# Performance work log

Hardware: AMD Instinct MI355X
Metric: run time of the kernel (lower is better)

The kernel has to match this reference:

```python
import jax, jax.numpy as jnp
import numpy as np

N_Q = 5000
MEM = 50
KDIM = 50
VDIM = 200
FC = 50
B = 2048
S = 200


def setup_inputs() -> dict:
    key = jax.random.key(0)
    ks = jax.random.split(key, 14)
    inp = {}
    inp["q_data"] = jax.random.randint(ks[0], (B, S), 0, N_Q, dtype=jnp.int64)
    inp["qa_data"] = jax.random.randint(ks[1], (B, S), 0, 2 * N_Q, dtype=jnp.int64)
    # learned parameters (kaiming-ish random init)
    inp["q_embed_w"] = jax.random.normal(ks[2], (N_Q + 1, KDIM), jnp.float32) * 0.2
    inp["qa_embed_w"] = jax.random.normal(ks[3], (2 * N_Q + 1, VDIM), jnp.float32) * 0.1
    inp["key_memory"] = jax.random.normal(ks[4], (MEM, KDIM), jnp.float32) * 0.2
    inp["init_value_memory"] = jax.random.normal(ks[5], (MEM, VDIM), jnp.float32) * 0.1
    # DKVMN write gates: erase (sigmoid) and add (tanh) transforms of qa embedding
    inp["erase_w"] = jax.random.normal(ks[6], (VDIM, VDIM), jnp.float32) * 0.1
    inp["erase_b"] = jnp.zeros((VDIM,), jnp.float32)
    inp["add_w"] = jax.random.normal(ks[7], (VDIM, VDIM), jnp.float32) * 0.1
    inp["add_b"] = jnp.zeros((VDIM,), jnp.float32)
    # prediction MLP: Linear(VDIM+KDIM -> FC), Tanh, Linear(FC -> 1)
    inp["pred_w1"] = jax.random.normal(ks[8], (VDIM + KDIM, FC), jnp.float32) * 0.1
    inp["pred_b1"] = jnp.zeros((FC,), jnp.float32)
    inp["pred_w2"] = jax.random.normal(ks[9], (FC, 1), jnp.float32) * 0.2
    inp["pred_b2"] = jnp.zeros((1,), jnp.float32)
    return inp


def _dkvmn_forward(q_data, qa_data, q_embed_w, qa_embed_w, key_memory,
                   init_value_memory, erase_w, erase_b, add_w, add_b,
                   pred_w1, pred_b1, pred_w2, pred_b2):
    q_emb = q_embed_w[q_data]    # [B, S, KDIM]
    qa_emb = qa_embed_w[qa_data]  # [B, S, VDIM]
    batch = q_data.shape[0]
    Mv0 = jnp.broadcast_to(init_value_memory, (batch, MEM, VDIM))

    def step(Mv, xs):
        q_t, qa_t = xs  # [B, KDIM], [B, VDIM]
        # attention over memory slots
        w = jax.nn.softmax(q_t @ key_memory.T, axis=-1)          # [B, MEM]
        read = jnp.einsum('bm,bmv->bv', w, Mv)                    # [B, VDIM]
        h = jnp.tanh(jnp.concatenate([read, q_t], -1) @ pred_w1 + pred_b1)
        p = jax.nn.sigmoid((h @ pred_w2 + pred_b2)[:, 0])         # [B]
        # erase/add write
        e = jax.nn.sigmoid(qa_t @ erase_w + erase_b)              # [B, VDIM]
        a = jnp.tanh(qa_t @ add_w + add_b)                        # [B, VDIM]
        Mv_new = Mv * (1.0 - w[:, :, None] * e[:, None, :]) + w[:, :, None] * a[:, None, :]
        return Mv_new, p

    xs = (jnp.swapaxes(q_emb, 0, 1), jnp.swapaxes(qa_emb, 0, 1))  # time-major
    _, preds = jax.lax.scan(step, Mv0, xs)                        # [S, B]
    return preds.T                                                # [B, S]


def reference(q_data, qa_data, q_embed_w, qa_embed_w, key_memory,
              init_value_memory, erase_w, erase_b, add_w, add_b,
              pred_w1, pred_b1, pred_w2, pred_b2):
    preds = _dkvmn_forward(q_data, qa_data, q_embed_w, qa_embed_w, key_memory,
                           init_value_memory, erase_w, erase_b, add_w, add_b,
                           pred_w1, pred_b1, pred_w2, pred_b2)
    zeros = jnp.zeros_like(preds)
    return (preds, zeros, zeros, zeros)
```

## Files before the change

### kernel.cpp

```cpp
#include <hip/hip_runtime.h>
#include <hip/hip_fp16.h>


#define NQ1   5001
#define NQA   10001
#define MEMN  50
#define KD    50
#define VD    200
#define FC    50
#define BB    2048
#define SS    200
#define EA_R  16
#define WHS   28

#define EA_B   626
#define WQ_B   1251
#define PACK_B 8
#define PREP_G (EA_B + WQ_B + PACK_B)

typedef unsigned int   u32;
typedef unsigned short u16;
typedef short    s8v __attribute__((ext_vector_type(8)));
typedef float    f4v __attribute__((ext_vector_type(4)));
typedef _Float16 h2v __attribute__((ext_vector_type(2)));

__device__ __forceinline__ float fast_sigmoid(float x) { return 1.f / (1.f + __expf(-x)); }
__device__ __forceinline__ float fast_tanh(float x) {
    float e2 = __expf(2.f * x);
    return 1.f - 2.f / (e2 + 1.f);
}
__device__ __forceinline__ float bfu16_to_f(u16 u) {
    union { float f; u32 i; } x; x.i = ((u32)u) << 16; return x.f;
}
__device__ __forceinline__ u16 f_to_bfu16(float f) {
    union { float f; u32 i; } x; x.f = f;
    return (u16)((x.i + 0x7fffu + ((x.i >> 16) & 1u)) >> 16);
}
__device__ __forceinline__ h2v u32_to_h2v(u32 u) {
    union { u32 i; h2v h; } x; x.i = u; return x.h;
}
__device__ __forceinline__ u16 f16bits(float f) {
    union { __half h; u16 u; } x; x.h = __float2half(f); return x.u;
}
__device__ __forceinline__ float h16_to_f(u16 u) {
    union { u16 u; __half h; } x; x.u = u; return __half2float(x.h);
}

__global__ __launch_bounds__(256) void prep(
        const float* __restrict__ qemb, const float* __restrict__ km,
        const float* __restrict__ w1,   const float* __restrict__ b1,
        const float* __restrict__ qaemb,
        const float* __restrict__ ew,   const float* __restrict__ ebias,
        const float* __restrict__ aw,   const float* __restrict__ abias,
        float* __restrict__ Wt, u32* __restrict__ Wh, float* __restrict__ Q1,
        u32* __restrict__ EA, u16* __restrict__ W1s,
        float* __restrict__ out_aux) {
    const int tid = threadIdx.x;
    const int blk = blockIdx.x;

    for (size_t i = (size_t)blk * 256 + tid; i < 3ull * BB * SS;
         i += (size_t)PREP_G * 256)
        out_aux[i] = 0.f;

    __shared__ float smem[VD * EA_R];

    if (blk < EA_B) {
        const int r0 = blk * EA_R;
        if (tid < VD) {
            #pragma unroll
            for (int r = 0; r < EA_R; ++r) {
                int row = r0 + r;
                smem[tid * EA_R + r] = (row < NQA) ? qaemb[(size_t)row * VD + tid] : 0.f;
            }
        }
        __syncthreads();
        if (tid >= VD) return;

        float accE[EA_R], accA[EA_R];
        #pragma unroll
        for (int r = 0; r < EA_R; ++r) { accE[r] = 0.f; accA[r] = 0.f; }
        for (int k = 0; k < VD; ++k) {
            float we = ew[k * VD + tid];
            float wa = aw[k * VD + tid];
            #pragma unroll
            for (int r = 0; r < EA_R; ++r) {
                float qv = smem[k * EA_R + r];
                accE[r] = fmaf(qv, we, accE[r]);
                accA[r] = fmaf(qv, wa, accA[r]);
            }
        }
        float be = ebias[tid], ba = abias[tid];
        #pragma unroll
        for (int r = 0; r < EA_R; ++r) {
            int row = r0 + r;
            if (row < NQA) {
                u16 ne16 = f16bits(-fast_sigmoid(accE[r] + be));
                u16 a16  = f16bits(fast_tanh(accA[r] + ba));
                EA[(size_t)row * VD + tid] = (u32)ne16 | ((u32)a16 << 16);
            }
        }
    } else if (blk < EA_B + WQ_B) {
        const int lane = tid & 63;
        const int wv   = tid >> 6;
        const int q    = (blk - EA_B) * 4 + wv;
        const bool qok = q < NQ1;
        float* qrow = smem + wv * 64;
        if (qok && lane < KD) qrow[lane] = qemb[q * KD + lane];
        __syncthreads();
        if (!qok) return;

        float s = -1e30f;
        if (lane < MEMN) {
            s = 0.f;
            #pragma unroll
            for (int k = 0; k < KD; ++k) s = fmaf(qrow[k], km[lane * KD + k], s);
        }
        float mx = s;
        #pragma unroll
        for (int off = 32; off >= 1; off >>= 1) mx = fmaxf(mx, __shfl_xor(mx, off, 64));
        float e = (lane < MEMN) ? __expf(s - mx) : 0.f;
        float sum = e;
        #pragma unroll
        for (int off = 32; off >= 1; off >>= 1) sum += __shfl_xor(sum, off, 64);
        float wv_ = (lane < MEMN) ? (e / sum) : 0.f;
        if (lane < MEMN) Wt[q * MEMN + lane] = wv_;

        float plo = __shfl(wv_, 2 * (lane & 31), 64);
        float phi = __shfl(wv_, 2 * (lane & 31) + 1, 64);
        if (lane < 25) {
            Wh[q * WHS + lane] = (u32)f16bits(plo) | ((u32)f16bits(phi) << 16);
        } else if (lane < WHS) {
            Wh[q * WHS + lane] = 0;
        }

        if (lane < FC) {
            float h = b1[lane];
            #pragma unroll
            for (int k = 0; k < KD; ++k)
                h = fmaf(qrow[k], w1[(VD + k) * FC + lane], h);
            Q1[q * FC + lane] = h;
        }
    } else {
        for (int idx = (blk - EA_B - WQ_B) * 256 + tid; idx < 4 * 7 * 64 * 8;
             idx += PACK_B * 256) {
            int j    = idx & 7;
            int lane = (idx >> 3) & 63;
            int kt   = (idx >> 9) % 7;
            int nt   = idx / 3584;
            int k = kt * 32 + ((lane >> 4) << 3) + j;
            int n = nt * 16 + (lane & 15);
            float v = (k < VD && n < FC) ? w1[k * FC + n] : 0.f;
            W1s[idx] = f_to_bfu16(v);
        }
    }
}

__global__ __launch_bounds__(256) void dkvmn_state(
        const int* __restrict__ qd, const int* __restrict__ qad,
        const u32* __restrict__ Wh, const u32* __restrict__ EA,
        const float* __restrict__ ivm, u16* __restrict__ READ) {
    const int tid = threadIdx.x;
    const int b   = blockIdx.x;
    const int v   = tid;
    const bool active = v < VD;
    const int vc = active ? v : VD - 1;

    h2v mv[25];
    #pragma unroll
    for (int i = 0; i < 25; ++i) {
        mv[i].x = (_Float16)ivm[(2 * i) * VD + vc];
        mv[i].y = (_Float16)ivm[(2 * i + 1) * VD + vc];
    }

    const int base = b * SS;
    int q_c = __builtin_amdgcn_readfirstlane(qd[base]);
    int q_n = __builtin_amdgcn_readfirstlane(qd[base + 1]);
    int qa0 = __builtin_amdgcn_readfirstlane(qad[base]);
    int qa1 = __builtin_amdgcn_readfirstlane(qad[base + 1]);
    u32 ea_c = EA[(size_t)qa0 * VD + vc];
    u32 ea_n = EA[(size_t)qa1 * VD + vc];

    for (int t = 0; t < SS; ++t) {
        int tn = t + 2; tn = (tn < SS) ? tn : (SS - 1);
        int q_nn  = __builtin_amdgcn_readfirstlane(qd[base + tn]);
        int qa_nn = __builtin_amdgcn_readfirstlane(qad[base + tn]);
        u32 ea_nn = EA[(size_t)qa_nn * VD + vc];

        const u32* wrow = Wh + q_c * WHS;
        h2v nev2 = u32_to_h2v(__builtin_amdgcn_perm(ea_c, ea_c, 0x01000100u));
        h2v av2  = u32_to_h2v(__builtin_amdgcn_perm(ea_c, ea_c, 0x03020302u));

        float rdA = 0.f, rdB = 0.f;
        #pragma unroll
        for (int i = 0; i < 25; i += 2) {
            h2v w0 = u32_to_h2v(wrow[i]);
#if __has_builtin(__builtin_amdgcn_fdot2)
            rdA = __builtin_amdgcn_fdot2(w0, mv[i], rdA, false);
#else
            rdA = fmaf((float)w0.x, (float)mv[i].x,
                  fmaf((float)w0.y, (float)mv[i].y, rdA));
#endif
            mv[i] = __builtin_elementwise_fma(
                w0, __builtin_elementwise_fma(nev2, mv[i], av2), mv[i]);
            if (i + 1 < 25) {
                h2v w1p = u32_to_h2v(wrow[i + 1]);
#if __has_builtin(__builtin_amdgcn_fdot2)
                rdB = __builtin_amdgcn_fdot2(w1p, mv[i + 1], rdB, false);
#else
                rdB = fmaf((float)w1p.x, (float)mv[i + 1].x,
                      fmaf((float)w1p.y, (float)mv[i + 1].y, rdB));
#endif
                mv[i + 1] = __builtin_elementwise_fma(
                    w1p, __builtin_elementwise_fma(nev2, mv[i + 1], av2), mv[i + 1]);
            }
        }
        if (active)
            READ[(size_t)(base + t) * VD + v] = f_to_bfu16(rdA + rdB);
        q_c = q_n; q_n = q_nn; ea_c = ea_n; ea_n = ea_nn;
    }
}

__global__ __launch_bounds__(256) void mlp_pred(
        const u16* __restrict__ RD, const int* __restrict__ qd,
        const float* __restrict__ Q1tab, const u16* __restrict__ W1s,
        const float* __restrict__ w2, const float* __restrict__ b2,
        float* __restrict__ out) {
    const int tid  = threadIdx.x;
    const int lane = tid & 63;
    const int wv   = tid >> 6;
    const int strip = blockIdx.x * 4 + wv;
    const int row0  = strip * 16;

    const int mrow = lane & 15;
    const int quad = lane >> 4;

    s8v a[7];
    {
        const u16* arow = RD + (size_t)(row0 + mrow) * VD + quad * 8;
        #pragma unroll
        for (int kt = 0; kt < 7; ++kt)
            a[kt] = *(const s8v*)(arow + kt * 32);
    }

    const float b2f = b2[0];
    float pf[4] = {0.f, 0.f, 0.f, 0.f};

    #pragma unroll
    for (int nt = 0; nt < 4; ++nt) {
        s8v bfr[7];
        #pragma unroll
        for (int kt = 0; kt < 7; ++kt)
            bfr[kt] = *(const s8v*)(W1s + (((nt * 7 + kt) * 64) + lane) * 8);

        f4v acc = {0.f, 0.f, 0.f, 0.f};
        #pragma unroll
        for (int kt = 0; kt < 7; ++kt)
            acc = __builtin_amdgcn_mfma_f32_16x16x32_bf16(a[kt], bfr[kt], acc, 0, 0, 0);

        const int f = nt * 16 + mrow;
        const float w2f = (f < FC) ? w2[f] : 0.f;
        #pragma unroll
        for (int r = 0; r < 4; ++r) {
            int row = row0 + quad * 4 + r;
            float h = acc[r] + Q1tab[qd[row] * FC + f];
            pf[r] = fmaf(fast_tanh(h), w2f, pf[r]);
        }
    }

    #pragma unroll
    for (int r = 0; r < 4; ++r) {
        float s = pf[r];
        s += __shfl_xor(s, 1, 64);
        s += __shfl_xor(s, 2, 64);
        s += __shfl_xor(s, 4, 64);
        s += __shfl_xor(s, 8, 64);
        if (mrow == 0)
            out[row0 + quad * 4 + r] = fast_sigmoid(s + b2f);
    }
}

__global__ void dkvmn_main(const int* __restrict__ qd, const int* __restrict__ qad,
                           const float* __restrict__ Wtab, const float* __restrict__ Q1tab,
                           const u32* __restrict__ EA,
                           const float* __restrict__ ivm,
                           const float* __restrict__ w1,
                           const float* __restrict__ w2,
                           const float* __restrict__ b2,
                           float* __restrict__ out) {
    const int tid  = threadIdx.x;
    const int b    = blockIdx.x;
    const int v    = tid;
    const int lane = tid & 63;
    const int wv   = tid >> 6;

    __shared__ alignas(16) float read_lds[4 * 52];
    __shared__ alignas(16) float part_lds[4 * 52];

    float mv[MEMN];
    if (v < VD) {
        #pragma unroll
        for (int m = 0; m < MEMN; ++m) mv[m] = ivm[m * VD + v];
    }
    float w1r[50];
    if (lane < FC) {
        #pragma unroll
        for (int i = 0; i < 50; ++i) w1r[i] = w1[(wv * 50 + i) * FC + lane];
    } else {
        #pragma unroll
        for (int i = 0; i < 50; ++i) w1r[i] = 0.f;
    }
    const float w2f = (tid < FC) ? w2[tid] : 0.f;
    const float b2f = b2[0];

    const int* qrow_i  = qd  + b * SS;
    const int* qarow_i = qad + b * SS;
    const int jchunk = v / 50;
    const int wslot  = jchunk * 52 + (v - jchunk * 50);

    for (int t = 0; t < SS; ++t) {
        const int q  = __builtin_amdgcn_readfirstlane(qrow_i[t]);
        const int qa = __builtin_amdgcn_readfirstlane(qarow_i[t]);
        const float* wrow = Wtab + q * MEMN;

        u32 ea = 0;
        if (v < VD) ea = EA[(size_t)qa * VD + v];
        float ne = h16_to_f((u16)(ea & 0xffffu));
        float av = h16_to_f((u16)(ea >> 16));

        if (v < VD) {
            float rd0 = 0.f, rd1 = 0.f;
            #pragma unroll
            for (int m = 0; m < MEMN; m += 2) {
                float wm0 = wrow[m], wm1 = wrow[m + 1];
                rd0 = fmaf(wm0, mv[m], rd0);
                mv[m] = fmaf(wm0, fmaf(ne, mv[m], av), mv[m]);
                rd1 = fmaf(wm1, mv[m + 1], rd1);
                mv[m + 1] = fmaf(wm1, fmaf(ne, mv[m + 1], av), mv[m + 1]);
            }
            read_lds[wslot] = rd0 + rd1;
        }
        __syncthreads();

        float part = 0.f;
        {
            const float* rlc = read_lds + wv * 52;
            #pragma unroll
            for (int i = 0; i < 48; i += 4) {
                float4 x = *(const float4*)(rlc + i);
                part = fmaf(x.x, w1r[i],     part);
                part = fmaf(x.y, w1r[i + 1], part);
                part = fmaf(x.z, w1r[i + 2], part);
                part = fmaf(x.w, w1r[i + 3], part);
            }
            part = fmaf(rlc[48], w1r[48], part);
            part = fmaf(rlc[49], w1r[49], part);
        }
        if (lane < FC) part_lds[wv * 52 + lane] = part;
        __syncthreads();

        if (wv == 0) {
            float pf = 0.f;
            if (lane < FC) {
                float h = part_lds[lane] + part_lds[52 + lane] +
                          part_lds[104 + lane] + part_lds[156 + lane] +
                          Q1tab[q * FC + lane];
                pf = fast_tanh(h) * w2f;
            }
            #pragma unroll
            for (int off = 32; off >= 1; off >>= 1) pf += __shfl_xor(pf, off, 64);
            if (lane == 0) out[b * SS + t] = fast_sigmoid(pf + b2f);
        }
    }
}

extern "C" void kernel_launch(void* const* d_in, const int* in_sizes, int n_in,
                              void* d_out, int out_size, void* d_ws, size_t ws_size,
                              hipStream_t stream) {
    const int* qd  = (const int*)d_in[0];
    const int* qad = (const int*)d_in[1];
    const float* qemb  = (const float*)d_in[2];
    const float* qaemb = (const float*)d_in[3];
    const float* km    = (const float*)d_in[4];
    const float* ivm   = (const float*)d_in[5];
    const float* ew    = (const float*)d_in[6];
    const float* eb    = (const float*)d_in[7];
    const float* aw    = (const float*)d_in[8];
    const float* ab    = (const float*)d_in[9];
    const float* w1    = (const float*)d_in[10];
    const float* b1    = (const float*)d_in[11];
    const float* w2    = (const float*)d_in[12];
    const float* b2    = (const float*)d_in[13];
    float* out = (float*)d_out;
    (void)in_sizes; (void)n_in; (void)out_size;

    char* ws = (char*)d_ws;
    float* Wt  = (float*)(ws);
    float* Q1  = (float*)(ws + 1000448);
    u32*   EA  = (u32*)  (ws + 2000896);
    u16*   W1s = (u16*)  (ws + 10001920);
    u32*   Wh  = (u32*)  (ws + 10034688);
    u16*   RD  = (u16*)  (ws + 10595328);
    const size_t need = 10595328ull + 163840000ull + 512ull;

    prep<<<PREP_G, 256, 0, stream>>>(qemb, km, w1, b1, qaemb, ew, eb, aw, ab,
                                     Wt, Wh, Q1, EA, W1s, out + (size_t)BB * SS);

    if (ws_size >= need) {
        dkvmn_state<<<BB, 256, 0, stream>>>(qd, qad, Wh, EA, ivm, RD);
        mlp_pred<<<(BB * SS) / 64, 256, 0, stream>>>(RD, qd, Q1, W1s, w2, b2, out);
    } else {
        dkvmn_main<<<BB, 256, 0, stream>>>(qd, qad, Wt, Q1, EA, ivm, w1, w2, b2, out);
    }
}
```

Measured before the change: 459.1 us.

## Split state kernel into single-wave blocks with split-slot tail wave

The recurrent memory-update kernel now launches four 64-thread blocks per batch element instead of one 256-thread block. Three waves each own 64 value columns, and a fourth wave handles the last 8 columns by splitting the 25 memory-slot pairs across 8 lane groups, combining partial reads with xor shuffles. The Wh row stride is padded from 28 to 32 so each lane group can load its weights as one aligned 128-bit vector, and the workspace offsets shift to match. The aim is to drop the idle fourth wave of the old layout and shorten the latency-bound serial chain for the tail columns, at the cost of more blocks and shuffle work.

```diff
diff --git a/kernel.cpp b/kernel.cpp
--- a/kernel.cpp
+++ b/kernel.cpp
@@ -11,7 +11,7 @@
 #define BB    2048
 #define SS    200
 #define EA_R  16
-#define WHS   28
+#define WHS   32
 
 #define EA_B   626
 #define WQ_B   1251
@@ -23,6 +23,7 @@
 typedef short    s8v __attribute__((ext_vector_type(8)));
 typedef float    f4v __attribute__((ext_vector_type(4)));
 typedef _Float16 h2v __attribute__((ext_vector_type(2)));
+typedef u32      u4v __attribute__((ext_vector_type(4)));
 
 __device__ __forceinline__ float fast_sigmoid(float x) { return 1.f / (1.f + __expf(-x)); }
 __device__ __forceinline__ float fast_tanh(float x) {
@@ -155,68 +156,129 @@
     }
 }
 
-__global__ __launch_bounds__(256) void dkvmn_state(
+__global__ __launch_bounds__(64) void dkvmn_state(
         const int* __restrict__ qd, const int* __restrict__ qad,
         const u32* __restrict__ Wh, const u32* __restrict__ EA,
         const float* __restrict__ ivm, u16* __restrict__ READ) {
-    const int tid = threadIdx.x;
-    const int b   = blockIdx.x;
-    const int v   = tid;
-    const bool active = v < VD;
-    const int vc = active ? v : VD - 1;
-
-    h2v mv[25];
-    #pragma unroll
-    for (int i = 0; i < 25; ++i) {
-        mv[i].x = (_Float16)ivm[(2 * i) * VD + vc];
-        mv[i].y = (_Float16)ivm[(2 * i + 1) * VD + vc];
-    }
-
+    const int tid  = threadIdx.x;
+    const int blk  = blockIdx.x;
+    const int b    = blk >> 2;
+    const int role = blk & 3;
     const int base = b * SS;
-    int q_c = __builtin_amdgcn_readfirstlane(qd[base]);
-    int q_n = __builtin_amdgcn_readfirstlane(qd[base + 1]);
-    int qa0 = __builtin_amdgcn_readfirstlane(qad[base]);
-    int qa1 = __builtin_amdgcn_readfirstlane(qad[base + 1]);
-    u32 ea_c = EA[(size_t)qa0 * VD + vc];
-    u32 ea_n = EA[(size_t)qa1 * VD + vc];
-
-    for (int t = 0; t < SS; ++t) {
-        int tn = t + 2; tn = (tn < SS) ? tn : (SS - 1);
-        int q_nn  = __builtin_amdgcn_readfirstlane(qd[base + tn]);
-        int qa_nn = __builtin_amdgcn_readfirstlane(qad[base + tn]);
-        u32 ea_nn = EA[(size_t)qa_nn * VD + vc];
-
-        const u32* wrow = Wh + q_c * WHS;
-        h2v nev2 = u32_to_h2v(__builtin_amdgcn_perm(ea_c, ea_c, 0x01000100u));
-        h2v av2  = u32_to_h2v(__builtin_amdgcn_perm(ea_c, ea_c, 0x03020302u));
-
-        float rdA = 0.f, rdB = 0.f;
-        #pragma unroll
-        for (int i = 0; i < 25; i += 2) {
-            h2v w0 = u32_to_h2v(wrow[i]);
+
+    if (role < 3) {
+        const int v = role * 64 + tid;
+
+        h2v mv[25];
+        #pragma unroll
+        for (int i = 0; i < 25; ++i) {
+            mv[i].x = (_Float16)ivm[(2 * i) * VD + v];
+            mv[i].y = (_Float16)ivm[(2 * i + 1) * VD + v];
+        }
+
+        int q_c = __builtin_amdgcn_readfirstlane(qd[base]);
+        int q_n = __builtin_amdgcn_readfirstlane(qd[base + 1]);
+        int qa0 = __builtin_amdgcn_readfirstlane(qad[base]);
+        int qa1 = __builtin_amdgcn_readfirstlane(qad[base + 1]);
+        u32 ea_c = EA[(size_t)qa0 * VD + v];
+        u32 ea_n = EA[(size_t)qa1 * VD + v];
+
+        for (int t = 0; t < SS; ++t) {
+            int tn = t + 2; tn = (tn < SS) ? tn : (SS - 1);
+            int q_nn  = __builtin_amdgcn_readfirstlane(qd[base + tn]);
+            int qa_nn = __builtin_amdgcn_readfirstlane(qad[base + tn]);
+            u32 ea_nn = EA[(size_t)qa_nn * VD + v];
+
+            const u32* wrow = Wh + q_c * WHS;
+            h2v nev2 = u32_to_h2v(__builtin_amdgcn_perm(ea_c, ea_c, 0x01000100u));
+            h2v av2  = u32_to_h2v(__builtin_amdgcn_perm(ea_c, ea_c, 0x03020302u));
+
+            float rdA = 0.f, rdB = 0.f;
+            #pragma unroll
+            for (int i = 0; i < 25; i += 2) {
+                h2v w0 = u32_to_h2v(wrow[i]);
 #if __has_builtin(__builtin_amdgcn_fdot2)
-            rdA = __builtin_amdgcn_fdot2(w0, mv[i], rdA, false);
+                rdA = __builtin_amdgcn_fdot2(w0, mv[i], rdA, false);
 #else
-            rdA = fmaf((float)w0.x, (float)mv[i].x,
-                  fmaf((float)w0.y, (float)mv[i].y, rdA));
+                rdA = fmaf((float)w0.x, (float)mv[i].x,
+                      fmaf((float)w0.y, (float)mv[i].y, rdA));
 #endif
-            mv[i] = __builtin_elementwise_fma(
-                w0, __builtin_elementwise_fma(nev2, mv[i], av2), mv[i]);
-            if (i + 1 < 25) {
-                h2v w1p = u32_to_h2v(wrow[i + 1]);
+                mv[i] = __builtin_elementwise_fma(
+                    w0, __builtin_elementwise_fma(nev2, mv[i], av2), mv[i]);
+                if (i + 1 < 25) {
+                    h2v w1p = u32_to_h2v(wrow[i + 1]);
 #if __has_builtin(__builtin_amdgcn_fdot2)
-                rdB = __builtin_amdgcn_fdot2(w1p, mv[i + 1], rdB, false);
+                    rdB = __builtin_amdgcn_fdot2(w1p, mv[i + 1], rdB, false);
 #else
-                rdB = fmaf((float)w1p.x, (float)mv[i + 1].x,
-                      fmaf((float)w1p.y, (float)mv[i + 1].y, rdB));
+                    rdB = fmaf((float)w1p.x, (float)mv[i + 1].x,
+                          fmaf((float)w1p.y, (float)mv[i + 1].y, rdB));
 #endif
-                mv[i + 1] = __builtin_elementwise_fma(
-                    w1p, __builtin_elementwise_fma(nev2, mv[i + 1], av2), mv[i + 1]);
-            }
-        }
-        if (active)
+                    mv[i + 1] = __builtin_elementwise_fma(
+                        w1p, __builtin_elementwise_fma(nev2, mv[i + 1], av2), mv[i + 1]);
+                }
+            }
             READ[(size_t)(base + t) * VD + v] = f_to_bfu16(rdA + rdB);
-        q_c = q_n; q_n = q_nn; ea_c = ea_n; ea_n = ea_nn;
+            q_c = q_n; q_n = q_nn; ea_c = ea_n; ea_n = ea_nn;
+        }
+    } else {
+        const int v8  = tid & 7;
+        const int grp = tid >> 3;
+        const int v   = 192 + v8;
+
+        h2v mv4[4];
+        #pragma unroll
+        for (int j = 0; j < 4; ++j) {
+            int p = grp * 4 + j;
+            if (p < 25) {
+                mv4[j].x = (_Float16)ivm[(2 * p) * VD + v];
+                mv4[j].y = (_Float16)ivm[(2 * p + 1) * VD + v];
+            } else {
+                mv4[j].x = (_Float16)0.f;
+                mv4[j].y = (_Float16)0.f;
+            }
+        }
+
+        int q_c = __builtin_amdgcn_readfirstlane(qd[base]);
+        int q_n = __builtin_amdgcn_readfirstlane(qd[base + 1]);
+        int qa0 = __builtin_amdgcn_readfirstlane(qad[base]);
+        int qa1 = __builtin_amdgcn_readfirstlane(qad[base + 1]);
+        u32 ea_c = EA[(size_t)qa0 * VD + v];
+        u32 ea_n = EA[(size_t)qa1 * VD + v];
+        u4v wq_c = *(const u4v*)(Wh + (size_t)q_c * WHS + grp * 4);
+        u4v wq_n = *(const u4v*)(Wh + (size_t)q_n * WHS + grp * 4);
+
+        for (int t = 0; t < SS; ++t) {
+            int tn = t + 2; tn = (tn < SS) ? tn : (SS - 1);
+            int q_nn  = __builtin_amdgcn_readfirstlane(qd[base + tn]);
+            int qa_nn = __builtin_amdgcn_readfirstlane(qad[base + tn]);
+            u32 ea_nn = EA[(size_t)qa_nn * VD + v];
+            u4v wq_nn = *(const u4v*)(Wh + (size_t)q_nn * WHS + grp * 4);
+
+            h2v nev2 = u32_to_h2v(__builtin_amdgcn_perm(ea_c, ea_c, 0x01000100u));
+            h2v av2  = u32_to_h2v(__builtin_amdgcn_perm(ea_c, ea_c, 0x03020302u));
+
+            float rd = 0.f;
+            #pragma unroll
+            for (int j = 0; j < 4; ++j) {
+                h2v w2 = u32_to_h2v(wq_c[j]);
+#if __has_builtin(__builtin_amdgcn_fdot2)
+                rd = __builtin_amdgcn_fdot2(w2, mv4[j], rd, false);
+#else
+                rd = fmaf((float)w2.x, (float)mv4[j].x,
+                     fmaf((float)w2.y, (float)mv4[j].y, rd));
+#endif
+                mv4[j] = __builtin_elementwise_fma(
+                    w2, __builtin_elementwise_fma(nev2, mv4[j], av2), mv4[j]);
+            }
+            rd += __shfl_xor(rd, 8, 64);
+            rd += __shfl_xor(rd, 16, 64);
+            rd += __shfl_xor(rd, 32, 64);
+            if (grp == 0)
+                READ[(size_t)(base + t) * VD + v] = f_to_bfu16(rd);
+
+            q_c = q_n; q_n = q_nn; ea_c = ea_n; ea_n = ea_nn;
+            wq_c = wq_n; wq_n = wq_nn;
+        }
     }
 }
 
@@ -399,14 +461,14 @@
     u32*   EA  = (u32*)  (ws + 2000896);
     u16*   W1s = (u16*)  (ws + 10001920);
     u32*   Wh  = (u32*)  (ws + 10034688);
-    u16*   RD  = (u16*)  (ws + 10595328);
-    const size_t need = 10595328ull + 163840000ull + 512ull;
+    u16*   RD  = (u16*)  (ws + 10675200);
+    const size_t need = 10675200ull + 163840000ull + 512ull;
 
     prep<<<PREP_G, 256, 0, stream>>>(qemb, km, w1, b1, qaemb, ew, eb, aw, ab,
                                      Wt, Wh, Q1, EA, W1s, out + (size_t)BB * SS);
 
     if (ws_size >= need) {
-        dkvmn_state<<<BB, 256, 0, stream>>>(qd, qad, Wh, EA, ivm, RD);
+        dkvmn_state<<<BB * 4, 64, 0, stream>>>(qd, qad, Wh, EA, ivm, RD);
         mlp_pred<<<(BB * SS) / 64, 256, 0, stream>>>(RD, qd, Q1, W1s, w2, b2, out);
     } else {
         dkvmn_main<<<BB, 256, 0, stream>>>(qd, qad, Wt, Q1, EA, ivm, w1, w2, b2, out);
```

New measurement: 459.0 us. Within noise of the previous version (-0.0%).
